# Kernel optimization log

Measured on AMD Instinct MI355X. Metric: run time of the kernel, lower is better.

The kernel has to match this reference:

```python
import jax, jax.numpy as jnp
import numpy as np

B, IN, CTX, OUT = 4096, 256, 64, 128
N, K, J = 128, 4, 64            # n_neurons, n_branches, branch_size (both layers)
NG = N * K                      # gates per layer = 512
WS = IN * NG                    # gating weight count per layer (gating always sees original x)
TP = 2 * (WS + NG)              # total hypernetwork output params = 263168
S = 0.05


def setup_inputs() -> dict:
    key = jax.random.key(0)
    ks = jax.random.split(key, 20)
    r = lambda i, shape: jax.random.normal(ks[i], shape, dtype=jnp.float32) * S
    return {
        "x": jax.random.normal(ks[0], (B, IN), dtype=jnp.float32),
        "context": jax.random.normal(ks[1], (CTX,), dtype=jnp.float32),
        # layer 0 (in=256): per-neuron per-branch linear + soma
        "Wb0": r(2, (N, K, J, IN)), "bb0": r(3, (N, K, J)),
        "Ws0": r(4, (N, K * J)),    "bs0": r(5, (N,)),
        # layer 1 (in=128)
        "Wb1": r(6, (N, K, J, N)),  "bb1": r(7, (N, K, J)),
        "Ws1": r(8, (N, K * J)),    "bs1": r(9, (N,)),
        # output layer
        "Wout": r(10, (OUT, N)), "bout": r(11, (OUT,)),
        # hypernetwork: ctx -> 32 -> 64 -> TP
        "h1w": r(12, (32, CTX)), "h1b": r(13, (32,)),
        "h2w": r(14, (64, 32)),  "h2b": r(15, (64,)),
        "h3w": r(16, (TP, 64)),  "h3b": r(17, (TP,)),
    }


def _dann_layer(cur, x, gw_slice, Wb, bb, Ws, bs):
    # gating weights derived from hypernetwork output vector (shared across batch)
    Wg = gw_slice[:WS].reshape(NG, IN)
    bg = gw_slice[WS:WS + NG]
    gates = jax.nn.sigmoid(x @ Wg.T + bg).reshape(-1, N, K, 1)      # [B,N,K,1]
    h = jax.nn.relu(jnp.einsum('bi,nkji->bnkj', cur, Wb) + bb) * gates
    return jnp.einsum('bnkj,nkj->bn', h, Ws.reshape(N, K, J)) + bs  # [B,N]


def reference(x, context, Wb0, bb0, Ws0, bs0, Wb1, bb1, Ws1, bs1,
              Wout, bout, h1w, h1b, h2w, h2b, h3w, h3b):
    # hypernetwork (dropout inactive at inference); single context -> one weight vector
    hv = jax.nn.relu(context @ h1w.T + h1b)
    hv = jax.nn.relu(hv @ h2w.T + h2b)
    gw = hv @ h3w.T + h3b                                           # [TP]
    per = WS + NG
    cur = _dann_layer(x,   x, gw[:per],        Wb0, bb0, Ws0, bs0)
    cur = _dann_layer(cur, x, gw[per:2 * per], Wb1, bb1, Ws1, bs1)
    return cur @ Wout.T + bout
```

## Files before the change

### kernel.cpp

```cpp
#include <hip/hip_runtime.h>

#define BB   4096
#define IN_  256
#define NN   128
#define KK   4
#define JJ   64
#define NG   512
#define WS_  131072
#define PER  131584
#define TP   263168
#define OUTD 128

typedef __attribute__((ext_vector_type(8))) short short8;
typedef __attribute__((ext_vector_type(4))) float f32x4;

__device__ __forceinline__ unsigned short f2bf(float f){
  unsigned u = __float_as_uint(f);
  return (unsigned short)((u + 0x7fffu + ((u >> 16) & 1u)) >> 16);
}

__device__ __forceinline__ void gload16(const void* g, void* l){
  __builtin_amdgcn_global_load_lds((const __attribute__((address_space(1))) void*)g,
                                   (__attribute__((address_space(3))) void*)l, 16, 0, 0);
}

#define XE  (4096u*256u)
#define W0E (XE + 8388608u)
#define W1E (W0E + 4194304u)

__global__ void k_convert(const float* __restrict__ x,
                          const float* __restrict__ w0,
                          const float* __restrict__ w1,
                          unsigned short* __restrict__ xb,
                          unsigned short* __restrict__ w0b,
                          unsigned short* __restrict__ w1b){
  size_t i = ((size_t)blockIdx.x*256 + threadIdx.x)*4;
  if (i >= W1E) return;
  const float* s; unsigned short* d; size_t off;
  if (i < XE)       { s = x;  d = xb;  off = i; }
  else if (i < W0E) { s = w0; d = w0b; off = i - XE; }
  else              { s = w1; d = w1b; off = i - W0E; }
  float4 v = *(const float4*)(s + off);
  ushort4 o;
  o.x = f2bf(v.x); o.y = f2bf(v.y); o.z = f2bf(v.z); o.w = f2bf(v.w);
  *(ushort4*)(d + off) = o;
}

__global__ void k_hyper(const float* __restrict__ ctx,
                        const float* __restrict__ h1w, const float* __restrict__ h1b,
                        const float* __restrict__ h2w, const float* __restrict__ h2b,
                        float* __restrict__ hv2){
  __shared__ float s1[32];
  int t = threadIdx.x;
  if (t < 32){
    float a = h1b[t];
    #pragma unroll 8
    for (int i = 0; i < 64; ++i) a += ctx[i]*h1w[t*64+i];
    s1[t] = fmaxf(a, 0.f);
  }
  __syncthreads();
  float a = h2b[t];
  #pragma unroll 8
  for (int i = 0; i < 32; ++i) a += s1[i]*h2w[t*32+i];
  hv2[t] = fmaxf(a, 0.f);
}

__global__ void k_gw(const float* __restrict__ hv2,
                     const float* __restrict__ h3w, const float* __restrict__ h3b,
                     unsigned short* __restrict__ Wg_bf, float* __restrict__ bg){
  int t = threadIdx.x;
  int r = blockIdx.x*64 + (t >> 2);
  int q = t & 3;
  const float4* row = (const float4*)(h3w + (size_t)r*64);
  float a = 0.f;
  #pragma unroll
  for (int i = 0; i < 4; ++i){
    float4 v = row[q*4 + i];
    float4 h = *(const float4*)(hv2 + q*16 + i*4);
    a += v.x*h.x + v.y*h.y + v.z*h.z + v.w*h.w;
  }
  a += __shfl_xor(a, 1);
  a += __shfl_xor(a, 2);
  if (q == 0){
    a += h3b[r];
    if (r < WS_)          Wg_bf[r] = f2bf(a);
    else if (r < PER)     bg[r - WS_] = a;
    else if (r < PER+WS_) Wg_bf[WS_ + (r - PER)] = f2bf(a);
    else                  bg[512 + (r - (PER+WS_))] = a;
  }
}

__global__ __launch_bounds__(512, 1)
void k_gates(const unsigned short* __restrict__ Wg_bf,
             const unsigned short* __restrict__ x_bf,
             const float* __restrict__ bg,
             float* __restrict__ GT){
  __shared__ __align__(16) unsigned short As[128*64];
  __shared__ __align__(16) unsigned short Bs[256*64];
  const int tid  = threadIdx.x;
  const int lane = tid & 63;
  const int wid  = tid >> 6;
  const int wm = wid >> 2, wn = wid & 3;
  const int lrow = lane & 15, lk = lane >> 4;
  const int m0 = blockIdx.x*128;
  const int b0 = blockIdx.y*256;

  f32x4 zero = {0.f,0.f,0.f,0.f};
  f32x4 acc[4][4];
  #pragma unroll
  for (int i=0;i<4;++i)
    #pragma unroll
    for (int j=0;j<4;++j) acc[i][j] = zero;

  for (int kt = 0; kt < 256/64; ++kt){
    __syncthreads();
    #pragma unroll
    for (int i = 0; i < 2; ++i){
      int c = tid + i*512;
      int row = c >> 3, k8 = c & 7;
      uint4 v = *(const uint4*)(Wg_bf + (size_t)(m0+row)*256 + kt*64 + k8*8);
      int idx = (row*64 + k8*8) ^ ((row & 7) << 3);
      *(uint4*)(&As[idx]) = v;
    }
    #pragma unroll
    for (int i = 0; i < 4; ++i){
      int c = tid + i*512;
      int row = c >> 3, k8 = c & 7;
      uint4 v = *(const uint4*)(x_bf + (size_t)(b0+row)*256 + kt*64 + k8*8);
      int idx = (row*64 + k8*8) ^ ((row & 7) << 3);
      *(uint4*)(&Bs[idx]) = v;
    }
    __syncthreads();
    #pragma unroll
    for (int kk = 0; kk < 2; ++kk){
      short8 a[4], b[4];
      #pragma unroll
      for (int fm = 0; fm < 4; ++fm){
        int m = wm*64 + fm*16 + lrow;
        int idx = (m*64 + kk*32 + lk*8) ^ ((m & 7) << 3);
        a[fm] = *(const short8*)(&As[idx]);
      }
      #pragma unroll
      for (int fn = 0; fn < 4; ++fn){
        int r = wn*64 + fn*16 + lrow;
        int idx = (r*64 + kk*32 + lk*8) ^ ((r & 7) << 3);
        b[fn] = *(const short8*)(&Bs[idx]);
      }
      #pragma unroll
      for (int fm = 0; fm < 4; ++fm)
        #pragma unroll
        for (int fn = 0; fn < 4; ++fn)
          acc[fm][fn] = __builtin_amdgcn_mfma_f32_16x16x32_bf16(a[fm], b[fn], acc[fm][fn], 0, 0, 0);
    }
  }
  #pragma unroll
  for (int fm = 0; fm < 4; ++fm){
    float4 bgv = *(const float4*)(bg + m0 + wm*64 + fm*16 + lk*4);
    float bga[4] = {bgv.x, bgv.y, bgv.z, bgv.w};
    #pragma unroll
    for (int reg = 0; reg < 4; ++reg){
      int m = m0 + wm*64 + fm*16 + lk*4 + reg;
      #pragma unroll
      for (int fn = 0; fn < 4; ++fn){
        int b = b0 + wn*64 + fn*16 + lrow;
        float z = acc[fm][fn][reg] + bga[reg];
        GT[(size_t)m*4096 + b] = 1.f/(1.f + __expf(-z));
      }
    }
  }
}

template<int KIN, int LAYER>
__global__ __launch_bounds__(512, 1)
void k_layer(const unsigned short* __restrict__ Abf,
             const unsigned short* __restrict__ Wbf,
             const float* __restrict__ bb,
             const float* __restrict__ Ws,
             const float* __restrict__ GT,
             float* __restrict__ partg){
  constexpr int NT = KIN/64;
  __shared__ __align__(16) unsigned short As[NT*8192];
  __shared__ __align__(16) unsigned short Bs[2][16384];

  const int tid  = threadIdx.x;
  const int lane = tid & 63;
  const int wid  = tid >> 6;
  const int wm = wid >> 2, wn = wid & 3;
  const int lrow = lane & 15, lk = lane >> 4;

  const int id     = blockIdx.x;
  const int nstart = (id & 7) * 16;
  const int bbase  = (id >> 3) << 7;

  f32x4 zero = {0.f,0.f,0.f,0.f};
  f32x4 acc[4][4];
  #pragma unroll
  for (int i=0;i<4;++i)
    #pragma unroll
    for (int jj=0;jj<4;++jj) acc[i][jj] = zero;

  auto STAGE_B = [&](int buf, int n, int kt){
    #pragma unroll
    for (int i = 0; i < 4; ++i){
      int c = i*512 + tid;
      int row = c >> 3, kc = c & 7;
      const unsigned short* s = Wbf + (size_t)((n<<8)+row)*KIN + kt*64 + ((kc ^ (row&7))<<3);
      gload16(s, &Bs[buf][(i*512 + wid*64)*8]);
    }
  };

  #pragma unroll
  for (int kt = 0; kt < NT; ++kt)
    #pragma unroll
    for (int i = 0; i < 2; ++i){
      int c = i*512 + tid;
      int row = c >> 3, kc = c & 7;
      const unsigned short* s = Abf + (size_t)(bbase+row)*KIN + kt*64 + ((kc ^ (row&7))<<3);
      gload16(s, &As[kt*8192 + (i*512 + wid*64)*8]);
    }
  STAGE_B(0, nstart, 0);
  asm volatile("" ::: "memory");

  int buf = 0;
  #pragma unroll 1
  for (int nn = 0; nn < 16; ++nn){
    const int n = nstart + nn;
    float4 gv[4];
    float bbv[4], wsv[4];
    #pragma unroll
    for (int kt = 0; kt < NT; ++kt){
      const bool epi  = (kt == NT-1);
      const bool last = epi && (nn == 15);

      if (nn == 0 && kt == 0)      asm volatile("s_waitcnt vmcnt(0)"  ::: "memory");
      else if (kt == 0)            asm volatile("s_waitcnt vmcnt(4)"  ::: "memory");
      else if (kt == 1)            asm volatile("s_waitcnt vmcnt(12)" ::: "memory");
      else                         asm volatile("s_waitcnt vmcnt(0)"  ::: "memory");
      __builtin_amdgcn_s_barrier();

      if (!last){
        int nb = n, nkt = kt + 1;
        if (nkt == NT){ nkt = 0; nb = n + 1; }
        STAGE_B(buf ^ 1, nb, nkt);
      }

      if (kt == 0){
        const int gidx = LAYER*512 + n*4 + wn;
        #pragma unroll
        for (int fm = 0; fm < 4; ++fm)
          gv[fm] = *(const float4*)(GT + (size_t)gidx*4096 + bbase + wm*64 + fm*16 + lk*4);
        #pragma unroll
        for (int fn = 0; fn < 4; ++fn){
          int c = wn*64 + fn*16 + lrow;
          bbv[fn] = bb[n*256 + c];
          wsv[fn] = Ws[n*256 + c];
        }
      }

      #pragma unroll
      for (int kk = 0; kk < 2; ++kk){
        short8 a[4], b[4];
        #pragma unroll
        for (int fm = 0; fm < 4; ++fm){
          int m = wm*64 + fm*16 + lrow;
          int idx = kt*8192 + ((m*64 + kk*32 + lk*8) ^ ((m & 7) << 3));
          a[fm] = *(const short8*)(&As[idx]);
        }
        #pragma unroll
        for (int fn = 0; fn < 4; ++fn){
          int r = wn*64 + fn*16 + lrow;
          int idx = (r*64 + kk*32 + lk*8) ^ ((r & 7) << 3);
          b[fn] = *(const short8*)(&Bs[buf][idx]);
        }
        #pragma unroll
        for (int fm = 0; fm < 4; ++fm)
          #pragma unroll
          for (int fn = 0; fn < 4; ++fn)
            acc[fm][fn] = __builtin_amdgcn_mfma_f32_16x16x32_bf16(a[fm], b[fn], acc[fm][fn], 0, 0, 0);
      }

      if (epi){
        #pragma unroll
        for (int fm = 0; fm < 4; ++fm){
          float gr[4] = {gv[fm].x, gv[fm].y, gv[fm].z, gv[fm].w};
          float sums[4];
          #pragma unroll
          for (int reg = 0; reg < 4; ++reg){
            float s = 0.f;
            #pragma unroll
            for (int fn = 0; fn < 4; ++fn)
              s += fmaxf(acc[fm][fn][reg] + bbv[fn], 0.f) * wsv[fn];
            s *= gr[reg];
            s += __shfl_xor(s, 1);
            s += __shfl_xor(s, 2);
            s += __shfl_xor(s, 4);
            s += __shfl_xor(s, 8);
            sums[reg] = s;
          }
          if (lrow == 0){
            float4 o; o.x = sums[0]; o.y = sums[1]; o.z = sums[2]; o.w = sums[3];
            *(float4*)(partg + (size_t)wn*524288 + (size_t)n*4096
                       + bbase + wm*64 + fm*16 + lk*4) = o;
          }
        }
        #pragma unroll
        for (int i2 = 0; i2 < 4; ++i2)
          #pragma unroll
          for (int j2 = 0; j2 < 4; ++j2) acc[i2][j2] = zero;
      }
      buf ^= 1;
    }
  }
}

template<int OUT_BF>
__global__ void k_mid(const float* __restrict__ partg, const float* __restrict__ bsv,
                      unsigned short* __restrict__ obf, float* __restrict__ of32){
  const int n = blockIdx.x;
  const int t = threadIdx.x;
  const float* p = partg + (size_t)n*4096 + t*16;
  const float bsn = bsv[n];
  #pragma unroll
  for (int i = 0; i < 4; ++i){
    float4 s0 = *(const float4*)(p + i*4);
    float4 s1 = *(const float4*)(p + 524288 + i*4);
    float4 s2 = *(const float4*)(p + 2*524288 + i*4);
    float4 s3 = *(const float4*)(p + 3*524288 + i*4);
    float v0 = ((s0.x + s1.x) + s2.x) + s3.x + bsn;
    float v1 = ((s0.y + s1.y) + s2.y) + s3.y + bsn;
    float v2 = ((s0.z + s1.z) + s2.z) + s3.z + bsn;
    float v3 = ((s0.w + s1.w) + s2.w) + s3.w + bsn;
    size_t b = (size_t)t*16 + i*4;
    if (OUT_BF){
      obf[(b+0)*128 + n] = f2bf(v0);
      obf[(b+1)*128 + n] = f2bf(v1);
      obf[(b+2)*128 + n] = f2bf(v2);
      obf[(b+3)*128 + n] = f2bf(v3);
    } else {
      of32[(b+0)*128 + n] = v0;
      of32[(b+1)*128 + n] = v1;
      of32[(b+2)*128 + n] = v2;
      of32[(b+3)*128 + n] = v3;
    }
  }
}

__global__ void k_final(const float* __restrict__ out1, const float* __restrict__ Wout,
                        const float* __restrict__ bout, float* __restrict__ out){
  int t = blockIdx.x*256 + threadIdx.x;
  int b = t >> 7, o = t & 127;
  const float4* cr = (const float4*)(out1 + (size_t)b*128);
  const float4* wr = (const float4*)(Wout + (size_t)o*128);
  float a = 0.f;
  #pragma unroll
  for (int i = 0; i < 32; ++i){
    float4 c = cr[i], w = wr[i];
    a += c.x*w.x + c.y*w.y + c.z*w.z + c.w*w.w;
  }
  out[t] = a + bout[o];
}

extern "C" void kernel_launch(void* const* d_in, const int* in_sizes, int n_in,
                              void* d_out, int out_size, void* d_ws, size_t ws_size,
                              hipStream_t stream){
  const float* x    = (const float*)d_in[0];
  const float* ctx  = (const float*)d_in[1];
  const float* Wb0  = (const float*)d_in[2];
  const float* bb0  = (const float*)d_in[3];
  const float* Ws0  = (const float*)d_in[4];
  const float* bs0  = (const float*)d_in[5];
  const float* Wb1  = (const float*)d_in[6];
  const float* bb1  = (const float*)d_in[7];
  const float* Ws1  = (const float*)d_in[8];
  const float* bs1  = (const float*)d_in[9];
  const float* Wout = (const float*)d_in[10];
  const float* bout = (const float*)d_in[11];
  const float* h1w  = (const float*)d_in[12];
  const float* h1b  = (const float*)d_in[13];
  const float* h2w  = (const float*)d_in[14];
  const float* h2b  = (const float*)d_in[15];
  const float* h3w  = (const float*)d_in[16];
  const float* h3b  = (const float*)d_in[17];
  float* out = (float*)d_out;

  char* ws = (char*)d_ws;
  size_t o = 0;
  unsigned short* x_bf  = (unsigned short*)(ws + o); o += (size_t)4096*256*2;
  unsigned short* W0b   = (unsigned short*)(ws + o); o += (size_t)8388608*2;
  unsigned short* W1b   = (unsigned short*)(ws + o); o += (size_t)4194304*2;
  unsigned short* Wg_bf = (unsigned short*)(ws + o); o += (size_t)1024*256*2;
  float* bg   = (float*)(ws + o); o += 1024*4;
  float* hv2  = (float*)(ws + o); o += 256;
  float* GT   = (float*)(ws + o); o += (size_t)1024*4096*4;
  unsigned short* cur_bf = (unsigned short*)(ws + o); o += (size_t)4096*128*2;
  float* out1 = (float*)(ws + o); o += (size_t)4096*128*4;
  float* partg0 = (float*)(ws + o); o += (size_t)4*128*4096*4;
  float* partg1 = (float*)W0b;

  k_convert<<<13312, 256, 0, stream>>>(x, Wb0, Wb1, x_bf, W0b, W1b);
  k_hyper<<<1, 64, 0, stream>>>(ctx, h1w, h1b, h2w, h2b, hv2);
  k_gw<<<4112, 256, 0, stream>>>(hv2, h3w, h3b, Wg_bf, bg);
  k_gates<<<dim3(8, 16), 512, 0, stream>>>(Wg_bf, x_bf, bg, GT);
  k_layer<256, 0><<<256, 512, 0, stream>>>(x_bf, W0b, bb0, Ws0, GT, partg0);
  k_mid<1><<<128, 256, 0, stream>>>(partg0, bs0, cur_bf, nullptr);
  k_layer<128, 1><<<256, 512, 0, stream>>>(cur_bf, W1b, bb1, Ws1, GT, partg1);
  k_mid<0><<<128, 256, 0, stream>>>(partg1, bs1, nullptr, out1);
  k_final<<<2048, 256, 0, stream>>>(out1, Wout, bout, out);
}
```

Baseline: 236.9 us.

## Triple-buffer weight tiles and hold activation fragments in registers

The layer kernel moves to one unified LDS array with three weight-tile buffers, prefetches two tiles ahead, and loads all activation MFMA fragments into registers once before the main loop. This removes per-iteration LDS reads of A and gives the asynchronous global-to-LDS weight loads more time to arrive, with vmcnt waits retuned to match. The gate, bias and soma-weight loads move into the epilogue. In exchange it uses much more register space (up to 64 short8 fragments for the 256-input layer), which risks spills or lower occupancy, and the hand-counted waits are fragile.

```diff
diff --git a/kernel.cpp b/kernel.cpp
--- a/kernel.cpp
+++ b/kernel.cpp
@@ -13,6 +13,8 @@
 
 typedef __attribute__((ext_vector_type(8))) short short8;
 typedef __attribute__((ext_vector_type(4))) float f32x4;
+
+#define VW(N) asm volatile("s_waitcnt vmcnt(" #N ")" ::: "memory")
 
 __device__ __forceinline__ unsigned short f2bf(float f){
   unsigned u = __float_as_uint(f);
@@ -178,9 +180,9 @@
              const float* __restrict__ Ws,
              const float* __restrict__ GT,
              float* __restrict__ partg){
-  constexpr int NT = KIN/64;
-  __shared__ __align__(16) unsigned short As[NT*8192];
-  __shared__ __align__(16) unsigned short Bs[2][16384];
+  constexpr int NT    = KIN/64;
+  constexpr int ABASE = (NT == 4) ? 32768 : 49152;
+  __shared__ __align__(16) unsigned short lds[65536];
 
   const int tid  = threadIdx.x;
   const int lane = tid & 63;
@@ -199,13 +201,13 @@
     #pragma unroll
     for (int jj=0;jj<4;++jj) acc[i][jj] = zero;
 
-  auto STAGE_B = [&](int buf, int n, int kt){
+  auto STAGE_B = [&](int sb, int n, int kt){
     #pragma unroll
     for (int i = 0; i < 4; ++i){
       int c = i*512 + tid;
       int row = c >> 3, kc = c & 7;
       const unsigned short* s = Wbf + (size_t)((n<<8)+row)*KIN + kt*64 + ((kc ^ (row&7))<<3);
-      gload16(s, &Bs[buf][(i*512 + wid*64)*8]);
+      gload16(s, &lds[sb*16384 + (i*512 + wid*64)*8]);
     }
   };
 
@@ -216,36 +218,73 @@
       int c = i*512 + tid;
       int row = c >> 3, kc = c & 7;
       const unsigned short* s = Abf + (size_t)(bbase+row)*KIN + kt*64 + ((kc ^ (row&7))<<3);
-      gload16(s, &As[kt*8192 + (i*512 + wid*64)*8]);
+      gload16(s, &lds[ABASE + kt*8192 + (i*512 + wid*64)*8]);
     }
   STAGE_B(0, nstart, 0);
+  STAGE_B(1, nstart, 1);
   asm volatile("" ::: "memory");
-
-  int buf = 0;
+  VW(8);
+  __builtin_amdgcn_s_barrier();
+
+  short8 areg[NT][2][4];
+  #pragma unroll
+  for (int kt = 0; kt < NT; ++kt)
+    #pragma unroll
+    for (int kk = 0; kk < 2; ++kk)
+      #pragma unroll
+      for (int fm = 0; fm < 4; ++fm){
+        int m = wm*64 + fm*16 + lrow;
+        int idx = ABASE + kt*8192 + ((m*64 + kk*32 + lk*8) ^ ((m & 7) << 3));
+        areg[kt][kk][fm] = *(const short8*)(&lds[idx]);
+      }
+  asm volatile("s_waitcnt lgkmcnt(0)" ::: "memory");
+  __builtin_amdgcn_s_barrier();
+
+  int cbuf = 0, sbuf = 2;
   #pragma unroll 1
   for (int nn = 0; nn < 16; ++nn){
     const int n = nstart + nn;
-    float4 gv[4];
-    float bbv[4], wsv[4];
     #pragma unroll
     for (int kt = 0; kt < NT; ++kt){
-      const bool epi  = (kt == NT-1);
-      const bool last = epi && (nn == 15);
-
-      if (nn == 0 && kt == 0)      asm volatile("s_waitcnt vmcnt(0)"  ::: "memory");
-      else if (kt == 0)            asm volatile("s_waitcnt vmcnt(4)"  ::: "memory");
-      else if (kt == 1)            asm volatile("s_waitcnt vmcnt(12)" ::: "memory");
-      else                         asm volatile("s_waitcnt vmcnt(0)"  ::: "memory");
+      const bool epi = (kt == NT-1);
+
+      if (NT == 4){
+        if (kt == 0){ if (nn == 0) VW(4); else VW(20); }
+        else if (kt == 1){ if (nn == 0) VW(4); else VW(20); }
+        else if (kt == 2){ VW(4); }
+        else { if (nn == 15) VW(0); else VW(4); }
+      } else {
+        if (kt == 0){ if (nn == 0) VW(4); else VW(20); }
+        else { if (nn == 0) VW(4); else if (nn == 15) VW(16); else VW(20); }
+      }
       __builtin_amdgcn_s_barrier();
 
-      if (!last){
-        int nb = n, nkt = kt + 1;
-        if (nkt == NT){ nkt = 0; nb = n + 1; }
-        STAGE_B(buf ^ 1, nb, nkt);
-      }
-
-      if (kt == 0){
+      if (!(nn == 15 && kt >= NT-2)){
+        int g2 = nn*NT + kt + 2;
+        STAGE_B(sbuf, nstart + g2/NT, g2 % NT);
+      }
+      asm volatile("" ::: "memory");
+
+      #pragma unroll
+      for (int kk = 0; kk < 2; ++kk){
+        short8 b[4];
+        #pragma unroll
+        for (int fn = 0; fn < 4; ++fn){
+          int r = wn*64 + fn*16 + lrow;
+          int idx = (r*64 + kk*32 + lk*8) ^ ((r & 7) << 3);
+          b[fn] = *(const short8*)(&lds[cbuf*16384 + idx]);
+        }
+        #pragma unroll
+        for (int fm = 0; fm < 4; ++fm)
+          #pragma unroll
+          for (int fn = 0; fn < 4; ++fn)
+            acc[fm][fn] = __builtin_amdgcn_mfma_f32_16x16x32_bf16(areg[kt][kk][fm], b[fn], acc[fm][fn], 0, 0, 0);
+      }
+
+      if (epi){
         const int gidx = LAYER*512 + n*4 + wn;
+        float4 gv[4];
+        float bbv[4], wsv[4];
         #pragma unroll
         for (int fm = 0; fm < 4; ++fm)
           gv[fm] = *(const float4*)(GT + (size_t)gidx*4096 + bbase + wm*64 + fm*16 + lk*4);
@@ -255,31 +294,6 @@
           bbv[fn] = bb[n*256 + c];
           wsv[fn] = Ws[n*256 + c];
         }
-      }
-
-      #pragma unroll
-      for (int kk = 0; kk < 2; ++kk){
-        short8 a[4], b[4];
-        #pragma unroll
-        for (int fm = 0; fm < 4; ++fm){
-          int m = wm*64 + fm*16 + lrow;
-          int idx = kt*8192 + ((m*64 + kk*32 + lk*8) ^ ((m & 7) << 3));
-          a[fm] = *(const short8*)(&As[idx]);
-        }
-        #pragma unroll
-        for (int fn = 0; fn < 4; ++fn){
-          int r = wn*64 + fn*16 + lrow;
-          int idx = (r*64 + kk*32 + lk*8) ^ ((r & 7) << 3);
-          b[fn] = *(const short8*)(&Bs[buf][idx]);
-        }
-        #pragma unroll
-        for (int fm = 0; fm < 4; ++fm)
-          #pragma unroll
-          for (int fn = 0; fn < 4; ++fn)
-            acc[fm][fn] = __builtin_amdgcn_mfma_f32_16x16x32_bf16(a[fm], b[fn], acc[fm][fn], 0, 0, 0);
-      }
-
-      if (epi){
         #pragma unroll
         for (int fm = 0; fm < 4; ++fm){
           float gr[4] = {gv[fm].x, gv[fm].y, gv[fm].z, gv[fm].w};
@@ -308,7 +322,8 @@
           #pragma unroll
           for (int j2 = 0; j2 < 4; ++j2) acc[i2][j2] = zero;
       }
-      buf ^= 1;
+      cbuf = (cbuf == 2) ? 0 : cbuf + 1;
+      sbuf = (sbuf == 2) ? 0 : sbuf + 1;
     }
   }
 }
```

After: 247.2 us. 4.3% more time.

## Make branch weights LDS-resident per block and stream activation tiles instead

Applied to the files above, without the earlier changes.

Flips the stationary operand of the dendritic-layer GEMM. Each block now owns one neuron's (or half a neuron's) branch weights, which are loaded into LDS once. Batch tiles of activations are double-buffered through LDS, replacing the old scheme that kept a batch tile resident and streamed weights for 16 neurons. Bias and soma weights are hoisted out of the loop, and the grid mapping and wait counts change to match. The aim is lower repeated weight traffic; in exchange, activation reads grow and the grid/LDS footprint shifts per layer.

```diff
diff --git a/kernel.cpp b/kernel.cpp
--- a/kernel.cpp
+++ b/kernel.cpp
@@ -13,6 +13,8 @@
 
 typedef __attribute__((ext_vector_type(8))) short short8;
 typedef __attribute__((ext_vector_type(4))) float f32x4;
+
+#define VW(N) asm volatile("s_waitcnt vmcnt(" #N ")" ::: "memory")
 
 __device__ __forceinline__ unsigned short f2bf(float f){
   unsigned u = __float_as_uint(f);
@@ -178,19 +180,30 @@
              const float* __restrict__ Ws,
              const float* __restrict__ GT,
              float* __restrict__ partg){
-  constexpr int NT = KIN/64;
-  __shared__ __align__(16) unsigned short As[NT*8192];
-  __shared__ __align__(16) unsigned short Bs[2][16384];
+  constexpr int NT     = KIN/64;
+  constexpr int SC     = (LAYER==0) ? 128 : 256;
+  constexpr int WN     = (LAYER==0) ? 2 : 4;
+  constexpr int WMN    = 8/WN;
+  constexpr int BTR    = WMN*64;
+  constexpr int NBT    = 16;
+  constexpr int ABUFSZ = BTR*64;
+  constexpr int WBOFF  = 2*ABUFSZ;
+  constexpr int AI     = BTR/64;
+  constexpr int WI     = SC/64;
+  __shared__ __align__(16) unsigned short lds[WBOFF + SC*64*NT];
 
   const int tid  = threadIdx.x;
   const int lane = tid & 63;
   const int wid  = tid >> 6;
-  const int wm = wid >> 2, wn = wid & 3;
+  const int wn   = wid % WN, wm = wid / WN;
   const int lrow = lane & 15, lk = lane >> 4;
 
-  const int id     = blockIdx.x;
-  const int nstart = (id & 7) * 16;
-  const int bbase  = (id >> 3) << 7;
+  const int id      = blockIdx.x;
+  const int n       = id >> 1;
+  const int sub     = id & 1;
+  const int kgrp    = (LAYER==0) ? sub*2 + wn : wn;
+  const int abase   = (LAYER==0) ? 0 : sub*2048;
+  const int colbase = n*256 + ((LAYER==0) ? sub*128 : 0);
 
   f32x4 zero = {0.f,0.f,0.f,0.f};
   f32x4 acc[4][4];
@@ -199,62 +212,64 @@
     #pragma unroll
     for (int jj=0;jj<4;++jj) acc[i][jj] = zero;
 
-  auto STAGE_B = [&](int buf, int n, int kt){
-    #pragma unroll
-    for (int i = 0; i < 4; ++i){
+  auto STAGE_A = [&](int buf, int bt, int kt){
+    #pragma unroll
+    for (int i = 0; i < AI; ++i){
       int c = i*512 + tid;
-      int row = c >> 3, kc = c & 7;
-      const unsigned short* s = Wbf + (size_t)((n<<8)+row)*KIN + kt*64 + ((kc ^ (row&7))<<3);
-      gload16(s, &Bs[buf][(i*512 + wid*64)*8]);
+      int r = c >> 3, kc = c & 7;
+      const unsigned short* s = Abf + (size_t)(abase + bt*BTR + r)*KIN + kt*64 + ((kc ^ (r&7))<<3);
+      gload16(s, &lds[buf*ABUFSZ + (i*512 + wid*64)*8]);
     }
   };
 
   #pragma unroll
   for (int kt = 0; kt < NT; ++kt)
     #pragma unroll
-    for (int i = 0; i < 2; ++i){
+    for (int i = 0; i < WI; ++i){
       int c = i*512 + tid;
-      int row = c >> 3, kc = c & 7;
-      const unsigned short* s = Abf + (size_t)(bbase+row)*KIN + kt*64 + ((kc ^ (row&7))<<3);
-      gload16(s, &As[kt*8192 + (i*512 + wid*64)*8]);
-    }
-  STAGE_B(0, nstart, 0);
+      int r = c >> 3, kc = c & 7;
+      const unsigned short* s = Wbf + (size_t)(colbase + r)*KIN + kt*64 + ((kc ^ (r&7))<<3);
+      gload16(s, &lds[WBOFF + kt*SC*64 + (i*512 + wid*64)*8]);
+    }
+  STAGE_A(0, 0, 0);
   asm volatile("" ::: "memory");
 
-  int buf = 0;
+  float bbv[4], wsv[4];
+  #pragma unroll
+  for (int fn = 0; fn < 4; ++fn){
+    int cloc = ((LAYER==0) ? sub*128 : 0) + wn*64 + fn*16 + lrow;
+    bbv[fn] = bb[n*256 + cloc];
+    wsv[fn] = Ws[n*256 + cloc];
+  }
+  const float* gtrow = GT + (size_t)(LAYER*512 + n*4 + kgrp)*4096 + abase;
+  float* prow = partg + (size_t)kgrp*524288 + (size_t)n*4096 + abase;
+
+  int abuf = 0;
   #pragma unroll 1
-  for (int nn = 0; nn < 16; ++nn){
-    const int n = nstart + nn;
+  for (int bt = 0; bt < NBT; ++bt){
     float4 gv[4];
-    float bbv[4], wsv[4];
     #pragma unroll
     for (int kt = 0; kt < NT; ++kt){
-      const bool epi  = (kt == NT-1);
-      const bool last = epi && (nn == 15);
-
-      if (nn == 0 && kt == 0)      asm volatile("s_waitcnt vmcnt(0)"  ::: "memory");
-      else if (kt == 0)            asm volatile("s_waitcnt vmcnt(4)"  ::: "memory");
-      else if (kt == 1)            asm volatile("s_waitcnt vmcnt(12)" ::: "memory");
-      else                         asm volatile("s_waitcnt vmcnt(0)"  ::: "memory");
+      const int  ph  = bt*NT + kt;
+      const bool epi = (kt == NT-1);
+
+      if (ph == 0)      VW(0);
+      else if (kt <= 1) VW(4);
+      else              VW(0);
       __builtin_amdgcn_s_barrier();
 
-      if (!last){
-        int nb = n, nkt = kt + 1;
-        if (nkt == NT){ nkt = 0; nb = n + 1; }
-        STAGE_B(buf ^ 1, nb, nkt);
-      }
+      if (ph + 1 < NBT*NT){
+        int bt2 = epi ? bt+1 : bt;
+        int kt2 = epi ? 0    : kt+1;
+        STAGE_A(abuf ^ 1, bt2, kt2);
+      }
+      asm volatile("" ::: "memory");
 
       if (kt == 0){
-        const int gidx = LAYER*512 + n*4 + wn;
         #pragma unroll
         for (int fm = 0; fm < 4; ++fm)
-          gv[fm] = *(const float4*)(GT + (size_t)gidx*4096 + bbase + wm*64 + fm*16 + lk*4);
-        #pragma unroll
-        for (int fn = 0; fn < 4; ++fn){
-          int c = wn*64 + fn*16 + lrow;
-          bbv[fn] = bb[n*256 + c];
-          wsv[fn] = Ws[n*256 + c];
-        }
+          gv[fm] = *(const float4*)(gtrow + bt*BTR + wm*64 + fm*16 + lk*4);
+        asm volatile("" ::: "memory");
       }
 
       #pragma unroll
@@ -263,14 +278,14 @@
         #pragma unroll
         for (int fm = 0; fm < 4; ++fm){
           int m = wm*64 + fm*16 + lrow;
-          int idx = kt*8192 + ((m*64 + kk*32 + lk*8) ^ ((m & 7) << 3));
-          a[fm] = *(const short8*)(&As[idx]);
+          int idx = abuf*ABUFSZ + ((m*64 + kk*32 + lk*8) ^ ((m & 7) << 3));
+          a[fm] = *(const short8*)(&lds[idx]);
         }
         #pragma unroll
         for (int fn = 0; fn < 4; ++fn){
           int r = wn*64 + fn*16 + lrow;
-          int idx = (r*64 + kk*32 + lk*8) ^ ((r & 7) << 3);
-          b[fn] = *(const short8*)(&Bs[buf][idx]);
+          int idx = WBOFF + kt*SC*64 + ((r*64 + kk*32 + lk*8) ^ ((r & 7) << 3));
+          b[fn] = *(const short8*)(&lds[idx]);
         }
         #pragma unroll
         for (int fm = 0; fm < 4; ++fm)
@@ -299,8 +314,7 @@
           }
           if (lrow == 0){
             float4 o; o.x = sums[0]; o.y = sums[1]; o.z = sums[2]; o.w = sums[3];
-            *(float4*)(partg + (size_t)wn*524288 + (size_t)n*4096
-                       + bbase + wm*64 + fm*16 + lk*4) = o;
+            *(float4*)(prow + bt*BTR + wm*64 + fm*16 + lk*4) = o;
           }
         }
         #pragma unroll
@@ -308,7 +322,7 @@
           #pragma unroll
           for (int j2 = 0; j2 < 4; ++j2) acc[i2][j2] = zero;
       }
-      buf ^= 1;
+      abuf ^= 1;
     }
   }
 }
```

Result: faster. 226.6 us (-4.3%).
